# Optimization experiments

Measured on AMD Instinct MI355X. Metric: run time of the kernel, lower is better.

Reference implementation:

```python
import jax, jax.numpy as jnp
import numpy as np

IN_FEATURES = 1024
OUT_FEATURES = 64   # per-head dim
NUM_HEADS = 16
DIM_PER_HEAD = IN_FEATURES // NUM_HEADS  # used for the 1/sqrt scale, per original code
B, S = 4, 1024


def setup_inputs() -> dict:
    key = jax.random.key(0)
    ks = jax.random.split(key, 12)
    HD = NUM_HEADS * OUT_FEATURES
    s = 1.0 / np.sqrt(IN_FEATURES)
    inp = {
        "q": jax.random.normal(ks[0], (B, S, IN_FEATURES), jnp.float32),
        "k": jax.random.normal(ks[1], (B, S, IN_FEATURES), jnp.float32),
        "v": jax.random.normal(ks[2], (B, S, IN_FEATURES), jnp.float32),
        "q_mask": jax.random.randint(ks[3], (B, S, 1), 0, 2).astype(jnp.float32),
        "k_mask": jax.random.randint(ks[4], (B, S, 1), 0, 2).astype(jnp.float32),
        "Wq": jax.random.normal(ks[5], (IN_FEATURES, HD), jnp.float32) * s,
        "bq": jnp.zeros((HD,), jnp.float32),
        "Wk": jax.random.normal(ks[6], (IN_FEATURES, HD), jnp.float32) * s,
        "bk": jnp.zeros((HD,), jnp.float32),
        "Wv": jax.random.normal(ks[7], (IN_FEATURES, HD), jnp.float32) * s,
        "bv": jnp.zeros((HD,), jnp.float32),
        "Wf": jax.random.normal(ks[8], (HD, IN_FEATURES), jnp.float32) * s,
        "bf": jnp.zeros((IN_FEATURES,), jnp.float32),
        "gamma": jnp.ones((IN_FEATURES,), jnp.float32),
        "beta": jnp.zeros((IN_FEATURES,), jnp.float32),
    }
    return inp


def _layer_norm(x, gamma, beta, eps=1e-5):
    mu = jnp.mean(x, axis=-1, keepdims=True)
    var = jnp.var(x, axis=-1, keepdims=True)
    return (x - mu) * jax.lax.rsqrt(var + eps) * gamma + beta


def reference(q, k, v, q_mask, k_mask, Wq, bq, Wk, bk, Wv, bv, Wf, bf, gamma, beta):
    residual = v
    Bs, Sq, _ = q.shape
    H, Do = NUM_HEADS, OUT_FEATURES
    # QKV projections, split heads: [B, H, S, Do]
    qh = (q @ Wq + bq).reshape(Bs, Sq, H, Do).transpose(0, 2, 1, 3)
    kh = (k @ Wk + bk).reshape(Bs, -1, H, Do).transpose(0, 2, 1, 3)
    vh = (v @ Wv + bv).reshape(Bs, -1, H, Do).transpose(0, 2, 1, 3)
    # custom mask: [B, Sq, Sk] via mask matmul, zero entries are invalid
    mask = jnp.einsum('bqm,bkm->bqk', q_mask, k_mask) / 300.0
    maskz = (mask == 0)[:, None, :, :]  # [B,1,Sq,Sk]
    # raw (unscaled) attention logits, returned as second output
    attention = jnp.einsum('bhqd,bhkd->bhqk', qh, kh)
    scores = attention / np.sqrt(DIM_PER_HEAD)
    scores = jnp.where(maskz, -1e9, scores)
    probs = jax.nn.softmax(scores, axis=-1)
    probs = jnp.where(maskz, 0.0, probs)
    context = jnp.einsum('bhqk,bhkd->bhqd', probs, vh)
    context = context.transpose(0, 2, 1, 3).reshape(Bs, Sq, H * Do)
    out = context @ Wf + bf  # dropout is identity (p=0 / eval)
    out = _layer_norm(out + residual, gamma, beta)
    return out, attention
```

## Files before the change

### kernel.cpp

```cpp
#include <hip/hip_runtime.h>
#include <hip/hip_bf16.h>
#include <stdint.h>


typedef __attribute__((ext_vector_type(8))) short v8s;
typedef __attribute__((ext_vector_type(4))) short v4s;
typedef __attribute__((ext_vector_type(4))) float v4f;

#define S_ 1024
#define MTOT 4096
#define LDA 72
#define LDP 136

__device__ __forceinline__ unsigned short f2b(float f) {
  union { float f; unsigned int u; } x; x.f = f;
  unsigned int u = x.u + 0x7fffu + ((x.u >> 16) & 1u);
  return (unsigned short)(u >> 16);
}

__global__ __launch_bounds__(256) void cast3_k(
    const float* __restrict__ q, const float* __restrict__ k, const float* __restrict__ v,
    unsigned short* __restrict__ qb, unsigned short* __restrict__ kb, unsigned short* __restrict__ vb) {
  const float* src = blockIdx.y == 0 ? q : blockIdx.y == 1 ? k : v;
  unsigned short* dst = blockIdx.y == 0 ? qb : blockIdx.y == 1 ? kb : vb;
  int i = (blockIdx.x * 256 + threadIdx.x) * 8;
  v4f a = *(const v4f*)(src + i);
  v4f b = *(const v4f*)(src + i + 4);
  union { unsigned short u[8]; v8s v; } o;
  o.u[0] = f2b(a[0]); o.u[1] = f2b(a[1]); o.u[2] = f2b(a[2]); o.u[3] = f2b(a[3]);
  o.u[4] = f2b(b[0]); o.u[5] = f2b(b[1]); o.u[6] = f2b(b[2]); o.u[7] = f2b(b[3]);
  *(v8s*)(dst + i) = o.v;
}

__global__ __launch_bounds__(256) void transpose_cast_k(
    const float* __restrict__ W0, const float* __restrict__ W1,
    const float* __restrict__ W2, const float* __restrict__ W3,
    unsigned short* __restrict__ T0, unsigned short* __restrict__ T1,
    unsigned short* __restrict__ T2, unsigned short* __restrict__ T3) {
  const float* W = blockIdx.z == 0 ? W0 : blockIdx.z == 1 ? W1 : blockIdx.z == 2 ? W2 : W3;
  unsigned short* T = blockIdx.z == 0 ? T0 : blockIdx.z == 1 ? T1 : blockIdx.z == 2 ? T2 : T3;
  __shared__ float tile[32][33];
  int tx = threadIdx.x & 31, ty = threadIdx.x >> 5;
  int n0 = blockIdx.x * 32, k0 = blockIdx.y * 32;
#pragma unroll
  for (int i = 0; i < 4; i++)
    tile[ty + i * 8][tx] = W[(size_t)(k0 + ty + i * 8) * 1024 + n0 + tx];
  __syncthreads();
#pragma unroll
  for (int i = 0; i < 4; i++)
    T[(size_t)(n0 + ty + i * 8) * 1024 + k0 + tx] = f2b(tile[tx][ty + i * 8]);
}

template <int MODE>
__global__ __launch_bounds__(256, 2) void gemm_k1024(
    const unsigned short* __restrict__ A, const unsigned short* __restrict__ Bt,
    const float* __restrict__ bias, void* __restrict__ Out) {
  __shared__ unsigned short As[128 * LDA];
  __shared__ unsigned short Bs[128 * LDA];
  const int t = threadIdx.x;
  const int wid = t >> 6, lane = t & 63;
  const int lrow = lane & 15, lquad = lane >> 4;
  const int m0 = blockIdx.x * 128, n0 = blockIdx.y * 128;
  const int wm = (wid & 1) * 64, wn = (wid >> 1) * 64;
  v4f zero = {0.f, 0.f, 0.f, 0.f};
  v4f acc[4][4];
#pragma unroll
  for (int i = 0; i < 4; i++)
#pragma unroll
    for (int j = 0; j < 4; j++) acc[i][j] = zero;

  for (int kt = 0; kt < 1024; kt += 64) {
    __syncthreads();
#pragma unroll
    for (int i = 0; i < 4; i++) {
      int c = t + i * 256;
      int r = c >> 3, col8 = (c & 7) * 8;
      *(v8s*)&As[r * LDA + col8] = *(const v8s*)&A[(size_t)(m0 + r) * 1024 + kt + col8];
      *(v8s*)&Bs[r * LDA + col8] = *(const v8s*)&Bt[(size_t)(n0 + r) * 1024 + kt + col8];
    }
    __syncthreads();
#pragma unroll
    for (int k32 = 0; k32 < 64; k32 += 32) {
      v8s af[4], bfv[4];
#pragma unroll
      for (int mi = 0; mi < 4; mi++)
        af[mi] = *(const v8s*)&As[(wm + mi * 16 + lrow) * LDA + k32 + lquad * 8];
#pragma unroll
      for (int ni = 0; ni < 4; ni++)
        bfv[ni] = *(const v8s*)&Bs[(wn + ni * 16 + lrow) * LDA + k32 + lquad * 8];
#pragma unroll
      for (int mi = 0; mi < 4; mi++)
#pragma unroll
        for (int ni = 0; ni < 4; ni++)
          acc[mi][ni] = __builtin_amdgcn_mfma_f32_16x16x32_bf16(af[mi], bfv[ni], acc[mi][ni], 0, 0, 0);
    }
  }
#pragma unroll
  for (int mi = 0; mi < 4; mi++) {
#pragma unroll
    for (int ni = 0; ni < 4; ni++) {
      int gn = n0 + wn + ni * 16 + lrow;
      float bv = bias[gn];
#pragma unroll
      for (int r = 0; r < 4; r++) {
        int gm = m0 + wm + mi * 16 + lquad * 4 + r;
        float val = acc[mi][ni][r] + bv;
        if (MODE == 0 || MODE == 1) {
          int b = gm >> 10, s = gm & 1023, h = gn >> 6, d = gn & 63;
          ((unsigned short*)Out)[(size_t)((b * 16 + h) * 1024 + s) * 64 + d] = f2b(val);
        } else if (MODE == 2) {
          int b = gm >> 10, s = gm & 1023, h = gn >> 6, d = gn & 63;
          ((unsigned short*)Out)[(size_t)((b * 16 + h) * 64 + d) * 1024 + s] = f2b(val);
        } else {
          ((float*)Out)[(size_t)gm * 1024 + gn] = val;
        }
      }
    }
  }
}

__global__ __launch_bounds__(256, 2) void attn_fused_k(
    const unsigned short* __restrict__ Qh, const unsigned short* __restrict__ Kh,
    const unsigned short* __restrict__ Vt,
    const float* __restrict__ q_mask, const float* __restrict__ k_mask,
    float* __restrict__ attn, unsigned short* __restrict__ ctx) {
  __shared__ __align__(16) unsigned short Ks[128 * LDA];
  __shared__ __align__(16) unsigned short Pl[4 * 32 * LDP];
  __shared__ __align__(16) float Sl[4 * 32];
  const int z = blockIdx.x, b = z >> 4, h = z & 15;
  const int q0 = blockIdx.y * 128;
  const int t = threadIdx.x, w = t >> 6, lane = t & 63;
  const int lrow = lane & 15, lq = lane >> 4;
  const unsigned short* Kz = Kh + (size_t)z * 1024 * 64;
  const unsigned short* Vz = Vt + (size_t)z * 64 * 1024;
  const float* km = k_mask + b * 1024;
  float* orow = attn + (size_t)z * 1024 * 1024;

  v8s qf[2][2];
#pragma unroll
  for (int ni = 0; ni < 2; ni++)
#pragma unroll
    for (int kb = 0; kb < 2; kb++)
      qf[ni][kb] = *(const v8s*)&Qh[((size_t)z * 1024 + q0 + w * 32 + ni * 16 + lrow) * 64 + kb * 32 + lq * 8];

  v4f zero = {0.f, 0.f, 0.f, 0.f};
  v4f acc_c[2][4];
#pragma unroll
  for (int i = 0; i < 2; i++)
#pragma unroll
    for (int j = 0; j < 4; j++) acc_c[i][j] = zero;
  float m_run[2] = {-1e30f, -1e30f};
  float l_run[2] = {0.f, 0.f};

  for (int kt = 0; kt < 8; kt++) {
    __syncthreads();
#pragma unroll
    for (int i = 0; i < 4; i++) {
      int c = t + i * 256, r = c >> 3, col8 = (c & 7) * 8;
      *(v8s*)&Ks[r * LDA + col8] = *(const v8s*)&Kz[(size_t)(kt * 128 + r) * 64 + col8];
    }
    __syncthreads();
    v4f sa[8][2];
#pragma unroll
    for (int mi = 0; mi < 8; mi++)
#pragma unroll
      for (int ni = 0; ni < 2; ni++) sa[mi][ni] = zero;
#pragma unroll
    for (int kb = 0; kb < 2; kb++) {
      v8s kf[8];
#pragma unroll
      for (int mi = 0; mi < 8; mi++)
        kf[mi] = *(const v8s*)&Ks[(mi * 16 + lrow) * LDA + kb * 32 + lq * 8];
#pragma unroll
      for (int mi = 0; mi < 8; mi++)
#pragma unroll
        for (int ni = 0; ni < 2; ni++)
          sa[mi][ni] = __builtin_amdgcn_mfma_f32_16x16x32_bf16(kf[mi], qf[ni][kb], sa[mi][ni], 0, 0, 0);
    }
#pragma unroll
    for (int mi = 0; mi < 8; mi++)
#pragma unroll
      for (int ni = 0; ni < 2; ni++)
        *(v4f*)&orow[(size_t)(q0 + w * 32 + ni * 16 + lrow) * 1024 + kt * 128 + mi * 16 + lq * 4] = sa[mi][ni];
    int msk[8];
#pragma unroll
    for (int mi = 0; mi < 8; mi++) {
      v4f kv = *(const v4f*)&km[kt * 128 + mi * 16 + lq * 4];
      msk[mi] = (kv[0] != 0.f ? 1 : 0) | (kv[1] != 0.f ? 2 : 0) |
                (kv[2] != 0.f ? 4 : 0) | (kv[3] != 0.f ? 8 : 0);
    }
#pragma unroll
    for (int ni = 0; ni < 2; ni++) {
      float tmax = -1e30f;
#pragma unroll
      for (int mi = 0; mi < 8; mi++)
#pragma unroll
        for (int r = 0; r < 4; r++)
          if ((msk[mi] >> r) & 1) tmax = fmaxf(tmax, sa[mi][ni][r] * 0.125f);
      tmax = fmaxf(tmax, __shfl_xor(tmax, 16));
      tmax = fmaxf(tmax, __shfl_xor(tmax, 32));
      float mnew = fmaxf(m_run[ni], tmax);
      float tsum = 0.f;
#pragma unroll
      for (int mi = 0; mi < 8; mi++) {
        v4s pk;
#pragma unroll
        for (int r = 0; r < 4; r++) {
          float p = ((msk[mi] >> r) & 1) ? __expf(sa[mi][ni][r] * 0.125f - mnew) : 0.f;
          pk[r] = (short)f2b(p);
          tsum += p;
        }
        *(v4s*)&Pl[(w * 32 + ni * 16 + lrow) * LDP + mi * 16 + lq * 4] = pk;
      }
      tsum += __shfl_xor(tsum, 16);
      tsum += __shfl_xor(tsum, 32);
      float sc = __expf(m_run[ni] - mnew);
      l_run[ni] = l_run[ni] * sc + tsum;
      m_run[ni] = mnew;
      if (lq == 0) Sl[w * 32 + ni * 16 + lrow] = sc;
    }
    asm volatile("s_waitcnt lgkmcnt(0)" ::: "memory");
    v4f sc0 = *(const v4f*)&Sl[w * 32 + lq * 4];
    v4f sc1 = *(const v4f*)&Sl[w * 32 + 16 + lq * 4];
#pragma unroll
    for (int nd = 0; nd < 4; nd++)
#pragma unroll
      for (int r = 0; r < 4; r++) {
        acc_c[0][nd][r] *= sc0[r];
        acc_c[1][nd][r] *= sc1[r];
      }
#pragma unroll
    for (int kk = 0; kk < 4; kk++) {
      v8s pa0 = *(const v8s*)&Pl[(w * 32 + lrow) * LDP + kk * 32 + lq * 8];
      v8s pa1 = *(const v8s*)&Pl[(w * 32 + 16 + lrow) * LDP + kk * 32 + lq * 8];
#pragma unroll
      for (int nd = 0; nd < 4; nd++) {
        v8s vb = *(const v8s*)&Vz[(size_t)(nd * 16 + lrow) * 1024 + kt * 128 + kk * 32 + lq * 8];
        acc_c[0][nd] = __builtin_amdgcn_mfma_f32_16x16x32_bf16(pa0, vb, acc_c[0][nd], 0, 0, 0);
        acc_c[1][nd] = __builtin_amdgcn_mfma_f32_16x16x32_bf16(pa1, vb, acc_c[1][nd], 0, 0, 0);
      }
    }
  }
  float qm0 = q_mask[b * 1024 + q0 + w * 32 + lrow];
  float qm1 = q_mask[b * 1024 + q0 + w * 32 + 16 + lrow];
  float r0 = (m_run[0] > -1e29f && l_run[0] > 0.f && qm0 != 0.f) ? (1.f / l_run[0]) : 0.f;
  float r1 = (m_run[1] > -1e29f && l_run[1] > 0.f && qm1 != 0.f) ? (1.f / l_run[1]) : 0.f;
  if (lq == 0) {
    Sl[w * 32 + lrow] = r0;
    Sl[w * 32 + 16 + lrow] = r1;
  }
  asm volatile("s_waitcnt lgkmcnt(0)" ::: "memory");
  v4f rc0 = *(const v4f*)&Sl[w * 32 + lq * 4];
  v4f rc1 = *(const v4f*)&Sl[w * 32 + 16 + lq * 4];
#pragma unroll
  for (int miq = 0; miq < 2; miq++)
#pragma unroll
    for (int nd = 0; nd < 4; nd++)
#pragma unroll
      for (int r = 0; r < 4; r++) {
        int s = q0 + w * 32 + miq * 16 + lq * 4 + r;
        int d = nd * 16 + lrow;
        float rr = (miq == 0) ? rc0[r] : rc1[r];
        ctx[((size_t)(b * 1024 + s)) * 1024 + h * 64 + d] = f2b(acc_c[miq][nd][r] * rr);
      }
}

__global__ __launch_bounds__(256) void resid_ln_k(
    const float* __restrict__ tmp, const float* __restrict__ resid,
    const float* __restrict__ gamma, const float* __restrict__ beta,
    float* __restrict__ out) {
  const int r = blockIdx.x, t = threadIdx.x;
  v4f x = *(const v4f*)(tmp + (size_t)r * 1024 + t * 4);
  v4f rv = *(const v4f*)(resid + (size_t)r * 1024 + t * 4);
  x = x + rv;
  float s = x[0] + x[1] + x[2] + x[3];
  float ss = x[0] * x[0] + x[1] * x[1] + x[2] * x[2] + x[3] * x[3];
#pragma unroll
  for (int off = 32; off; off >>= 1) { s += __shfl_xor(s, off); ss += __shfl_xor(ss, off); }
  __shared__ float red[8];
  const int wid = t >> 6, lane = t & 63;
  if (lane == 0) { red[wid] = s; red[4 + wid] = ss; }
  __syncthreads();
  s = red[0] + red[1] + red[2] + red[3];
  ss = red[4] + red[5] + red[6] + red[7];
  const float mu = s * (1.f / 1024.f);
  float var = ss * (1.f / 1024.f) - mu * mu;
  var = fmaxf(var, 0.f);
  const float rs = rsqrtf(var + 1e-5f);
  v4f g = *(const v4f*)(gamma + t * 4);
  v4f be = *(const v4f*)(beta + t * 4);
  v4f o = (x - mu) * rs * g + be;
  *(v4f*)(out + (size_t)r * 1024 + t * 4) = o;
}

extern "C" void kernel_launch(void* const* d_in, const int* in_sizes, int n_in,
                              void* d_out, int out_size, void* d_ws, size_t ws_size,
                              hipStream_t stream) {
  const float* q      = (const float*)d_in[0];
  const float* k      = (const float*)d_in[1];
  const float* v      = (const float*)d_in[2];
  const float* q_mask = (const float*)d_in[3];
  const float* k_mask = (const float*)d_in[4];
  const float* Wq = (const float*)d_in[5];
  const float* bq = (const float*)d_in[6];
  const float* Wk = (const float*)d_in[7];
  const float* bk = (const float*)d_in[8];
  const float* Wv = (const float*)d_in[9];
  const float* bv = (const float*)d_in[10];
  const float* Wf = (const float*)d_in[11];
  const float* bf = (const float*)d_in[12];
  const float* gamma = (const float*)d_in[13];
  const float* beta  = (const float*)d_in[14];

  float* out0 = (float*)d_out;
  float* attn = out0 + (size_t)MTOT * 1024;

  char* w = (char*)d_ws;
  const size_t MB = (size_t)1 << 20;
  unsigned short* qb  = (unsigned short*)(w + 0);
  unsigned short* kb  = (unsigned short*)(w + 8 * MB);
  unsigned short* vb  = (unsigned short*)(w + 16 * MB);
  unsigned short* WqT = (unsigned short*)(w + 24 * MB);
  unsigned short* WkT = (unsigned short*)(w + 26 * MB);
  unsigned short* WvT = (unsigned short*)(w + 28 * MB);
  unsigned short* WfT = (unsigned short*)(w + 30 * MB);
  unsigned short* Qh  = (unsigned short*)(w + 32 * MB);
  unsigned short* Kh  = (unsigned short*)(w + 40 * MB);
  unsigned short* Vt  = (unsigned short*)(w + 48 * MB);
  unsigned short* ctx = (unsigned short*)(w + 0);
  float* tmp          = (float*)(w + 8 * MB);

  cast3_k<<<dim3(2048, 3), 256, 0, stream>>>(q, k, v, qb, kb, vb);
  transpose_cast_k<<<dim3(32, 32, 4), 256, 0, stream>>>(Wq, Wk, Wv, Wf, WqT, WkT, WvT, WfT);
  gemm_k1024<0><<<dim3(32, 8), 256, 0, stream>>>(qb, WqT, bq, Qh);
  gemm_k1024<1><<<dim3(32, 8), 256, 0, stream>>>(kb, WkT, bk, Kh);
  gemm_k1024<2><<<dim3(32, 8), 256, 0, stream>>>(vb, WvT, bv, Vt);
  attn_fused_k<<<dim3(64, 8), 256, 0, stream>>>(Qh, Kh, Vt, q_mask, k_mask, attn, ctx);
  gemm_k1024<3><<<dim3(32, 8), 256, 0, stream>>>(ctx, WfT, bf, tmp);
  resid_ln_k<<<4096, 256, 0, stream>>>(tmp, v, gamma, beta, out0);
}
```

Baseline: 530.2 us.

## Merge QKV GEMMs, split-K output GEMM, use direct global-to-LDS loads

```diff
diff --git a/kernel.cpp b/kernel.cpp
--- a/kernel.cpp
+++ b/kernel.cpp
@@ -11,6 +11,11 @@
 #define MTOT 4096
 #define LDA 72
 #define LDP 136
+
+#define GLD16(gp, lp)                                                              \
+  __builtin_amdgcn_global_load_lds(                                                \
+      (const __attribute__((address_space(1))) unsigned int*)(gp),                 \
+      (__attribute__((address_space(3))) unsigned int*)(lp), 16, 0, 0)
 
 __device__ __forceinline__ unsigned short f2b(float f) {
   union { float f; unsigned int u; } x; x.f = f;
@@ -51,12 +56,21 @@
     T[(size_t)(n0 + ty + i * 8) * 1024 + k0 + tx] = f2b(tile[tx][ty + i * 8]);
 }
 
-template <int MODE>
-__global__ __launch_bounds__(256, 2) void gemm_k1024(
-    const unsigned short* __restrict__ A, const unsigned short* __restrict__ Bt,
-    const float* __restrict__ bias, void* __restrict__ Out) {
-  __shared__ unsigned short As[128 * LDA];
-  __shared__ unsigned short Bs[128 * LDA];
+__global__ __launch_bounds__(256, 2) void qkv_gemm_k(
+    const unsigned short* __restrict__ qb, const unsigned short* __restrict__ kb,
+    const unsigned short* __restrict__ vb,
+    const unsigned short* __restrict__ WqT, const unsigned short* __restrict__ WkT,
+    const unsigned short* __restrict__ WvT,
+    const float* __restrict__ bq, const float* __restrict__ bk, const float* __restrict__ bv,
+    unsigned short* __restrict__ Qh, unsigned short* __restrict__ Kh,
+    unsigned short* __restrict__ Vt) {
+  __shared__ __align__(16) unsigned short As[128 * 64];
+  __shared__ __align__(16) unsigned short Bs[128 * 64];
+  const int z = blockIdx.z;
+  const unsigned short* A  = z == 0 ? qb : z == 1 ? kb : vb;
+  const unsigned short* Bt = z == 0 ? WqT : z == 1 ? WkT : WvT;
+  const float* bias        = z == 0 ? bq : z == 1 ? bk : bv;
+  unsigned short* Out      = z == 0 ? Qh : z == 1 ? Kh : Vt;
   const int t = threadIdx.x;
   const int wid = t >> 6, lane = t & 63;
   const int lrow = lane & 15, lquad = lane >> 4;
@@ -75,8 +89,8 @@
     for (int i = 0; i < 4; i++) {
       int c = t + i * 256;
       int r = c >> 3, col8 = (c & 7) * 8;
-      *(v8s*)&As[r * LDA + col8] = *(const v8s*)&A[(size_t)(m0 + r) * 1024 + kt + col8];
-      *(v8s*)&Bs[r * LDA + col8] = *(const v8s*)&Bt[(size_t)(n0 + r) * 1024 + kt + col8];
+      GLD16(&A[(size_t)(m0 + r) * 1024 + kt + col8], &As[c * 8]);
+      GLD16(&Bt[(size_t)(n0 + r) * 1024 + kt + col8], &Bs[c * 8]);
     }
     __syncthreads();
 #pragma unroll
@@ -84,10 +98,10 @@
       v8s af[4], bfv[4];
 #pragma unroll
       for (int mi = 0; mi < 4; mi++)
-        af[mi] = *(const v8s*)&As[(wm + mi * 16 + lrow) * LDA + k32 + lquad * 8];
+        af[mi] = *(const v8s*)&As[(wm + mi * 16 + lrow) * 64 + k32 + lquad * 8];
 #pragma unroll
       for (int ni = 0; ni < 4; ni++)
-        bfv[ni] = *(const v8s*)&Bs[(wn + ni * 16 + lrow) * LDA + k32 + lquad * 8];
+        bfv[ni] = *(const v8s*)&Bs[(wn + ni * 16 + lrow) * 64 + k32 + lquad * 8];
 #pragma unroll
       for (int mi = 0; mi < 4; mi++)
 #pragma unroll
@@ -100,23 +114,77 @@
 #pragma unroll
     for (int ni = 0; ni < 4; ni++) {
       int gn = n0 + wn + ni * 16 + lrow;
-      float bv = bias[gn];
+      float bv_ = bias[gn];
 #pragma unroll
       for (int r = 0; r < 4; r++) {
         int gm = m0 + wm + mi * 16 + lquad * 4 + r;
-        float val = acc[mi][ni][r] + bv;
-        if (MODE == 0 || MODE == 1) {
-          int b = gm >> 10, s = gm & 1023, h = gn >> 6, d = gn & 63;
-          ((unsigned short*)Out)[(size_t)((b * 16 + h) * 1024 + s) * 64 + d] = f2b(val);
-        } else if (MODE == 2) {
-          int b = gm >> 10, s = gm & 1023, h = gn >> 6, d = gn & 63;
-          ((unsigned short*)Out)[(size_t)((b * 16 + h) * 64 + d) * 1024 + s] = f2b(val);
-        } else {
-          ((float*)Out)[(size_t)gm * 1024 + gn] = val;
-        }
+        float val = acc[mi][ni][r] + bv_;
+        int b = gm >> 10, s = gm & 1023, h = gn >> 6, d = gn & 63;
+        if (z < 2)
+          Out[(size_t)((b * 16 + h) * 1024 + s) * 64 + d] = f2b(val);
+        else
+          Out[(size_t)((b * 16 + h) * 64 + d) * 1024 + s] = f2b(val);
       }
     }
   }
+}
+
+__global__ __launch_bounds__(256, 2) void fgemm_k(
+    const unsigned short* __restrict__ A, const unsigned short* __restrict__ Bt,
+    float* __restrict__ tmp0, float* __restrict__ tmp1) {
+  __shared__ __align__(16) unsigned short As[128 * 64];
+  __shared__ __align__(16) unsigned short Bs[128 * 64];
+  const int z = blockIdx.z;
+  float* Out = z == 0 ? tmp0 : tmp1;
+  const int t = threadIdx.x;
+  const int wid = t >> 6, lane = t & 63;
+  const int lrow = lane & 15, lquad = lane >> 4;
+  const int m0 = blockIdx.x * 128, n0 = blockIdx.y * 128;
+  const int wm = (wid & 1) * 64, wn = (wid >> 1) * 64;
+  v4f zero = {0.f, 0.f, 0.f, 0.f};
+  v4f acc[4][4];
+#pragma unroll
+  for (int i = 0; i < 4; i++)
+#pragma unroll
+    for (int j = 0; j < 4; j++) acc[i][j] = zero;
+
+  for (int kt = z * 512; kt < z * 512 + 512; kt += 64) {
+    __syncthreads();
+#pragma unroll
+    for (int i = 0; i < 4; i++) {
+      int c = t + i * 256;
+      int r = c >> 3, col8 = (c & 7) * 8;
+      GLD16(&A[(size_t)(m0 + r) * 1024 + kt + col8], &As[c * 8]);
+      GLD16(&Bt[(size_t)(n0 + r) * 1024 + kt + col8], &Bs[c * 8]);
+    }
+    __syncthreads();
+#pragma unroll
+    for (int k32 = 0; k32 < 64; k32 += 32) {
+      v8s af[4], bfv[4];
+#pragma unroll
+      for (int mi = 0; mi < 4; mi++)
+        af[mi] = *(const v8s*)&As[(wm + mi * 16 + lrow) * 64 + k32 + lquad * 8];
+#pragma unroll
+      for (int ni = 0; ni < 4; ni++)
+        bfv[ni] = *(const v8s*)&Bs[(wn + ni * 16 + lrow) * 64 + k32 + lquad * 8];
+#pragma unroll
+      for (int mi = 0; mi < 4; mi++)
+#pragma unroll
+        for (int ni = 0; ni < 4; ni++)
+          acc[mi][ni] = __builtin_amdgcn_mfma_f32_16x16x32_bf16(af[mi], bfv[ni], acc[mi][ni], 0, 0, 0);
+    }
+  }
+#pragma unroll
+  for (int mi = 0; mi < 4; mi++)
+#pragma unroll
+    for (int ni = 0; ni < 4; ni++) {
+      int gn = n0 + wn + ni * 16 + lrow;
+#pragma unroll
+      for (int r = 0; r < 4; r++) {
+        int gm = m0 + wm + mi * 16 + lquad * 4 + r;
+        Out[(size_t)gm * 1024 + gn] = acc[mi][ni][r];
+      }
+    }
 }
 
 __global__ __launch_bounds__(256, 2) void attn_fused_k(
@@ -266,13 +334,16 @@
 }
 
 __global__ __launch_bounds__(256) void resid_ln_k(
-    const float* __restrict__ tmp, const float* __restrict__ resid,
+    const float* __restrict__ tmp0, const float* __restrict__ tmp1,
+    const float* __restrict__ bf, const float* __restrict__ resid,
     const float* __restrict__ gamma, const float* __restrict__ beta,
     float* __restrict__ out) {
   const int r = blockIdx.x, t = threadIdx.x;
-  v4f x = *(const v4f*)(tmp + (size_t)r * 1024 + t * 4);
+  v4f x0 = *(const v4f*)(tmp0 + (size_t)r * 1024 + t * 4);
+  v4f x1 = *(const v4f*)(tmp1 + (size_t)r * 1024 + t * 4);
+  v4f bv = *(const v4f*)(bf + t * 4);
   v4f rv = *(const v4f*)(resid + (size_t)r * 1024 + t * 4);
-  x = x + rv;
+  v4f x = x0 + x1 + bv + rv;
   float s = x[0] + x[1] + x[2] + x[3];
   float ss = x[0] * x[0] + x[1] * x[1] + x[2] * x[2] + x[3] * x[3];
 #pragma unroll
@@ -328,14 +399,13 @@
   unsigned short* Kh  = (unsigned short*)(w + 40 * MB);
   unsigned short* Vt  = (unsigned short*)(w + 48 * MB);
   unsigned short* ctx = (unsigned short*)(w + 0);
-  float* tmp          = (float*)(w + 8 * MB);
+  float* tmp0         = (float*)(w + 8 * MB);
+  float* tmp1         = (float*)(w + 32 * MB);
 
   cast3_k<<<dim3(2048, 3), 256, 0, stream>>>(q, k, v, qb, kb, vb);
   transpose_cast_k<<<dim3(32, 32, 4), 256, 0, stream>>>(Wq, Wk, Wv, Wf, WqT, WkT, WvT, WfT);
-  gemm_k1024<0><<<dim3(32, 8), 256, 0, stream>>>(qb, WqT, bq, Qh);
-  gemm_k1024<1><<<dim3(32, 8), 256, 0, stream>>>(kb, WkT, bk, Kh);
-  gemm_k1024<2><<<dim3(32, 8), 256, 0, stream>>>(vb, WvT, bv, Vt);
+  qkv_gemm_k<<<dim3(32, 8, 3), 256, 0, stream>>>(qb, kb, vb, WqT, WkT, WvT, bq, bk, bv, Qh, Kh, Vt);
   attn_fused_k<<<dim3(64, 8), 256, 0, stream>>>(Qh, Kh, Vt, q_mask, k_mask, attn, ctx);
-  gemm_k1024<3><<<dim3(32, 8), 256, 0, stream>>>(ctx, WfT, bf, tmp);
-  resid_ln_k<<<4096, 256, 0, stream>>>(tmp, v, gamma, beta, out0);
-}
+  fgemm_k<<<dim3(32, 8, 2), 256, 0, stream>>>(ctx, WfT, tmp0, tmp1);
+  resid_ln_k<<<4096, 256, 0, stream>>>(tmp0, tmp1, bf, v, gamma, beta, out0);
+}
```

New measurement: 482.8 us. 8.9% less time.
